# Optimization experiments

Measured on AMD Instinct MI355X. Metric: run time of the kernel, lower is better.

## Reference

```python
import jax, jax.numpy as jnp
import numpy as np
from itertools import combinations

H_RANK_MAX = 2
SELF_TP_RANK_MAX = 2
BASIS_RANK_MAX = 2
N_NODES = 25000
N_EDGES = 200000
N_CHANNELS = 32
DIM = 3
LETTERS = 'abdfghijklmn'  # avoid 'e' (edge) and 'c' (channel)


def _pairings(idxs):
    # all perfect matchings of a list of leg positions
    if not idxs:
        yield []
        return
    a = idxs[0]
    for i in range(1, len(idxs)):
        rest = idxs[1:i] + idxs[i + 1:]
        for p in _pairings(rest):
            yield [(a, idxs[i])] + p


def _contraction_subs(n_in, n_out):
    # all ways to keep n_out free legs (order-preserving) and pair up the rest
    specs = []
    for free in combinations(range(n_in), n_out):
        rest = [i for i in range(n_in) if i not in free]
        for match in _pairings(rest):
            sub = [None] * n_in
            out = ''
            li = 0
            for f in free:
                sub[f] = LETTERS[li]; out += LETTERS[li]; li += 1
            for x, y in match:
                sub[x] = sub[y] = LETTERS[li]; li += 1
            specs.append((''.join(sub), out))
    return specs


def _find_combinations(a_max, b_max, s):
    if s > a_max + b_max or s < 0:
        return []
    return [(a, s - a) for a in range(max(0, s - b_max), min(a_max, s) + 1)]


def setup_inputs() -> dict:
    key = jax.random.key(0)
    ks = jax.random.split(key, 9)
    return {
        'h0': jax.random.normal(ks[0], (N_NODES, N_CHANNELS), dtype=jnp.float32),
        'h1': jax.random.normal(ks[1], (N_NODES, N_CHANNELS, DIM), dtype=jnp.float32),
        'h2': jax.random.normal(ks[2], (N_NODES, N_CHANNELS, DIM, DIM), dtype=jnp.float32),
        'rel_pos': jax.random.normal(ks[3], (N_EDGES, DIM), dtype=jnp.float32),
        'edge_attr0': jax.random.normal(ks[4], (N_EDGES,), dtype=jnp.float32),
        'edge_attr1': jax.random.normal(ks[5], (N_EDGES, DIM), dtype=jnp.float32),
        'edge_attr2': jax.random.normal(ks[6], (N_EDGES, DIM, DIM), dtype=jnp.float32),
        'channel_weights': jax.random.normal(ks[7], (H_RANK_MAX + 1, N_CHANNELS, N_CHANNELS), dtype=jnp.float32),
        'edge_index': jax.random.randint(ks[8], (2, N_EDGES), 0, N_NODES, dtype=jnp.int64 if jax.config.jax_enable_x64 else jnp.int32),
    }


def _forward(h0, h1, h2, edge_attr0, edge_attr1, edge_attr2, channel_weights, edge_index):
    h = [h0, h1, h2]
    attr = [edge_attr0, edge_attr1, edge_attr2]
    recv = edge_index[1]
    # gather per-edge features and mix channels: [E, C, 3^r]
    h = [jnp.einsum('ij,kj...->ki...', channel_weights[r], h[r][recv])
         for r in range(H_RANK_MAX + 1)]
    acc = [None] * (BASIS_RANK_MAX + 1)
    for n_idx in range(H_RANK_MAX + SELF_TP_RANK_MAX + 1):
        for a, b in _find_combinations(H_RANK_MAX, SELF_TP_RANK_MAX, n_idx):
            for br in range(BASIS_RANK_MAX + 1):
                if n_idx >= br and (n_idx - br) % 2 == 0:
                    for sub, out in _contraction_subs(n_idx, br):
                        # contract outer(h[a], attr[b]) down to br free Cartesian legs
                        t = jnp.einsum(f'ec{sub[:a]},e{sub[a:]}->ec{out}', h[a], attr[b])
                        acc[br] = t if acc[br] is None else acc[br] + t
    send = edge_index[0]
    # scatter-sum per-edge messages into nodes
    return tuple(jax.ops.segment_sum(acc[br], send, num_segments=N_NODES)
                 for br in range(BASIS_RANK_MAX + 1))


def reference(h0, h1, h2, rel_pos, edge_attr0, edge_attr1, edge_attr2, channel_weights, edge_index):
    # rel_pos is accepted (matches original forward signature) but unused by the math
    return _forward(h0, h1, h2, edge_attr0, edge_attr1, edge_attr2, channel_weights, edge_index)
```

## Files before the change

kernel.cpp:

```cpp
#include <hip/hip_runtime.h>

#define N_NODES 25000
#define N_EDGES 200000
#define NC 32
#define DMAX 64

typedef unsigned int u32;
typedef u32   u32x4 __attribute__((ext_vector_type(4)));
typedef u32   u32x2 __attribute__((ext_vector_type(2)));
typedef float f32x2 __attribute__((ext_vector_type(2)));
typedef float f32x4 __attribute__((ext_vector_type(4)));
typedef u32x4 u32x4_a4 __attribute__((aligned(4)));
typedef u32x2 u32x2_a4 __attribute__((aligned(4)));
typedef f32x2 f32x2_a4 __attribute__((aligned(4)));
typedef f32x4 f32x4_a4 __attribute__((aligned(4)));

static constexpr size_t HM_BYTES   = (size_t)N_NODES * NC * 28;
static constexpr size_t SLOTS_OFF  = HM_BYTES;
static constexpr size_t CURSOR_OFF = SLOTS_OFF + (size_t)N_NODES * DMAX * 8;
static constexpr size_t WS_NEEDED  = CURSOR_OFF + (size_t)N_NODES * 4;

__device__ __forceinline__ unsigned short f2b(float f) {
    union { float f; unsigned u; } v; v.f = f;
    unsigned r = v.u + 0x7FFFu + ((v.u >> 16) & 1u);
    return (unsigned short)(r >> 16);
}
__device__ __forceinline__ float blo(u32 u) { return __uint_as_float(u << 16); }
__device__ __forceinline__ float bhi(u32 u) { return __uint_as_float(u & 0xFFFF0000u); }

__device__ __forceinline__ void edge_contract_g(
    float G, const float H1v[3], const float H2v[9],
    float a0, const float a1[3], const float a2[9],
    float& acc0, float acc1[3], float acc2[9])
{
    const float t2 = a2[0] + a2[4] + a2[8];
    const float s  = a0 + t2;

    float sA[9], S2[9];
#pragma unroll
    for (int a = 0; a < 3; ++a)
#pragma unroll
        for (int b = 0; b < 3; ++b) {
            sA[a*3+b] = a2[a*3+b] + a2[b*3+a];
            S2[a*3+b] = H2v[a*3+b] + H2v[b*3+a];
        }

    float v0 = G * s;
#pragma unroll
    for (int a = 0; a < 3; ++a) v0 += H1v[a] * a1[a];
#pragma unroll
    for (int k = 0; k < 9; ++k) v0 += H2v[k] * sA[k];
    acc0 += v0;

#pragma unroll
    for (int a = 0; a < 3; ++a) {
        float v = G * a1[a] + H1v[a] * s;
#pragma unroll
        for (int b = 0; b < 3; ++b)
            v += sA[a*3+b] * H1v[b] + S2[a*3+b] * a1[b];
        acc1[a] += v;
    }

#pragma unroll
    for (int a = 0; a < 3; ++a)
#pragma unroll
        for (int b = 0; b < 3; ++b) {
            float v = G * a2[a*3+b] + H1v[a] * a1[b] + H2v[a*3+b] * s;
#pragma unroll
            for (int d = 0; d < 3; ++d)
                v += S2[a*3+d] * sA[d*3+b];
            acc2[a*3+b] += v;
        }
}

__device__ __forceinline__ void edge_contract(
    float H0v, const float H1v[3], const float H2v[9],
    float a0, const float a1[3], const float a2[9],
    float& acc0, float acc1[3], float acc2[9])
{
    const float T2 = H2v[0] + H2v[4] + H2v[8];
    edge_contract_g(H0v + T2, H1v, H2v, a0, a1, a2, acc0, acc1, acc2);
}

__global__ __launch_bounds__(256) void mixscatter_kernel(
    const float* __restrict__ h0, const float* __restrict__ h1,
    const float* __restrict__ h2, const float* __restrict__ W,
    const int* __restrict__ ei,
    char* __restrict__ Hm, int2* __restrict__ slots, int* __restrict__ cursor)
{
    const int tid = threadIdx.x;

    if (blockIdx.x >= 3125) {
        const int e = (blockIdx.x - 3125) * 256 + tid;
        if (e < N_EDGES) {
            const int send = ei[e];
            const int pos  = atomicAdd(&cursor[send], 1);
            if (pos < DMAX) {
                int2 sl; sl.x = e; sl.y = ei[N_EDGES + e];
                slots[send * DMAX + pos] = sl;
            }
        }
        return;
    }

    __shared__ float Wt[3 * 32 * 32];
    __shared__ __align__(16) float h_lds[8 * 512];

    const int n0 = blockIdx.x * 8;

#pragma unroll
    for (int k = 0; k < 12; ++k) {
        int q = tid + k * 256;
        int r = q >> 10;
        int j = (q >> 5) & 31;
        int i = q & 31;
        Wt[q] = W[r * 1024 + i * 32 + j];
    }

    {
        int idx = tid;
        h_lds[(idx >> 5) * 512 + (idx & 31) * 16 + 0] = h0[(size_t)n0 * 32 + idx];
    }
#pragma unroll
    for (int k = 0; k < 3; ++k) {
        int idx = tid + k * 256;
        int ln = idx / 96, rem = idx % 96;
        h_lds[ln * 512 + (rem / 3) * 16 + 1 + (rem % 3)] = h1[(size_t)n0 * 96 + idx];
    }
#pragma unroll
    for (int k = 0; k < 9; ++k) {
        int idx = tid + k * 256;
        int ln = idx / 288, rem = idx % 288;
        h_lds[ln * 512 + (rem / 9) * 16 + 4 + (rem % 9)] = h2[(size_t)n0 * 288 + idx];
    }
    __syncthreads();

    const int ln = tid >> 5;
    const int i  = tid & 31;
    const int n  = n0 + ln;

    float acc[13];
#pragma unroll
    for (int p = 0; p < 13; ++p) acc[p] = 0.f;

#pragma unroll 4
    for (int j = 0; j < 32; ++j) {
        const float w0 = Wt[          j * 32 + i];
        const float w1 = Wt[1024 +    j * 32 + i];
        const float w2 = Wt[2048 +    j * 32 + i];
        const float* hv = &h_lds[ln * 512 + j * 16];
        const f32x4 qa = *(const f32x4*)(hv);
        const f32x4 qb = *(const f32x4*)(hv + 4);
        const f32x4 qc = *(const f32x4*)(hv + 8);
        const float hc = hv[12];
        acc[0]  += w0 * qa.x;
        acc[1]  += w1 * qa.y;  acc[2]  += w1 * qa.z;  acc[3]  += w1 * qa.w;
        acc[4]  += w2 * qb.x;  acc[5]  += w2 * qb.y;  acc[6]  += w2 * qb.z;
        acc[7]  += w2 * qb.w;  acc[8]  += w2 * qc.x;  acc[9]  += w2 * qc.y;
        acc[10] += w2 * qc.z;  acc[11] += w2 * qc.w;  acc[12] += w2 * hc;
    }

    acc[0] += acc[4] + acc[8] + acc[12];

    unsigned short b[13];
#pragma unroll
    for (int p = 0; p < 13; ++p) b[p] = f2b(acc[p]);
    u32 w0 = (u32)b[0]  | ((u32)b[1]  << 16);
    u32 w1 = (u32)b[2]  | ((u32)b[3]  << 16);
    u32 w2 = (u32)b[4]  | ((u32)b[5]  << 16);
    u32 w3 = (u32)b[6]  | ((u32)b[7]  << 16);
    u32 w4 = (u32)b[8]  | ((u32)b[9]  << 16);
    u32 w5 = (u32)b[10] | ((u32)b[11] << 16);
    u32 w6 = (u32)b[12];

    char* dst = Hm + (size_t)n * 896 + i * 28;
    u32x4 q0; q0.x = w0; q0.y = w1; q0.z = w2; q0.w = w3;
    u32x2 q1; q1.x = w4; q1.y = w5;
    *(u32x4_a4*)dst        = q0;
    *(u32x2_a4*)(dst + 16) = q1;
    *(u32*)(dst + 24)      = w6;
}

__global__ __launch_bounds__(128) void gather_kernel(
    const char* __restrict__ Hm, const int2* __restrict__ slots,
    const int* __restrict__ cursor,
    const float* __restrict__ ea0, const float* __restrict__ ea1,
    const float* __restrict__ ea2,
    float* __restrict__ out0, float* __restrict__ out1, float* __restrict__ out2)
{
    const int n    = blockIdx.x * 2 + (threadIdx.x >> 6);
    const int lane = threadIdx.x & 63;
    const int c    = lane & 31;
    const int par  = lane >> 5;

    const int draw = cursor[n];
    const int d    = draw < DMAX ? draw : DMAX;
    const int2* sb = slots + (u32)n * DMAX;
    const u32 c28  = (u32)c * 28u;

    const int2 my_sl = sb[lane];

    float acc0 = 0.f, acc1[3] = {0.f, 0.f, 0.f};
    float acc2[9] = {0.f, 0.f, 0.f, 0.f, 0.f, 0.f, 0.f, 0.f, 0.f};

#pragma unroll 2
    for (int i = par; i < d; i += 2) {
        const u32 e    = (u32)__shfl(my_sl.x, i);
        const u32 recv = (u32)__shfl(my_sl.y, i);

        const char* hmp = Hm + (recv * 896u + c28);
        const u32x4 q0 = *(const u32x4_a4*)hmp;
        const u32x2 q1 = *(const u32x2_a4*)(hmp + 16);
        const u32   q2 = *(const u32*)(hmp + 24);

        const float Gv = blo(q0.x);
        float H1v[3], H2v[9];
        H1v[0] = bhi(q0.x); H1v[1] = blo(q0.y); H1v[2] = bhi(q0.y);
        H2v[0] = blo(q0.z); H2v[1] = bhi(q0.z); H2v[2] = blo(q0.w);
        H2v[3] = bhi(q0.w); H2v[4] = blo(q1.x); H2v[5] = bhi(q1.x);
        H2v[6] = blo(q1.y); H2v[7] = bhi(q1.y); H2v[8] = blo(q2);

        const float a0 = ea0[e];
        float a1[3], a2[9];
        {
            const f32x2 v = *(const f32x2_a4*)(ea1 + e * 3u);
            a1[0] = v.x; a1[1] = v.y; a1[2] = ea1[e * 3u + 2u];
            const f32x4 b0 = *(const f32x4_a4*)(ea2 + e * 9u);
            const f32x4 b1 = *(const f32x4_a4*)(ea2 + e * 9u + 4u);
            a2[0] = b0.x; a2[1] = b0.y; a2[2] = b0.z; a2[3] = b0.w;
            a2[4] = b1.x; a2[5] = b1.y; a2[6] = b1.z; a2[7] = b1.w;
            a2[8] = ea2[e * 9u + 8u];
        }

        edge_contract_g(Gv, H1v, H2v, a0, a1, a2, acc0, acc1, acc2);
    }

    acc0 += __shfl_xor(acc0, 32);
#pragma unroll
    for (int a = 0; a < 3; ++a) acc1[a] += __shfl_xor(acc1[a], 32);
#pragma unroll
    for (int k = 0; k < 9; ++k) acc2[k] += __shfl_xor(acc2[k], 32);

    if (par == 0) {
        const u32 base = (u32)n * 32u + (u32)c;
        out0[base] = acc0;
        f32x2 o1; o1.x = acc1[0]; o1.y = acc1[1];
        *(f32x2_a4*)(out1 + base * 3u) = o1;
        out1[base * 3u + 2u] = acc1[2];
        f32x4 oa; oa.x = acc2[0]; oa.y = acc2[1]; oa.z = acc2[2]; oa.w = acc2[3];
        f32x4 ob; ob.x = acc2[4]; ob.y = acc2[5]; ob.z = acc2[6]; ob.w = acc2[7];
        *(f32x4_a4*)(out2 + base * 9u)      = oa;
        *(f32x4_a4*)(out2 + base * 9u + 4u) = ob;
        out2[base * 9u + 8u] = acc2[8];
    }
}

__global__ __launch_bounds__(256) void fused_edge_kernel(
    const float* __restrict__ h0, const float* __restrict__ h1,
    const float* __restrict__ h2, const float* __restrict__ W,
    const float* __restrict__ ea0, const float* __restrict__ ea1,
    const float* __restrict__ ea2, const int* __restrict__ ei,
    float* __restrict__ out0, float* __restrict__ out1, float* __restrict__ out2)
{
    __shared__ float Wt[3 * 32 * 32];
    __shared__ float h_lds[8 * 417];

    const int tid = threadIdx.x;
#pragma unroll
    for (int k = 0; k < 12; ++k) {
        int q = tid + k * 256;
        int r = q >> 10;
        int j = (q >> 5) & 31;
        int i = q & 31;
        Wt[q] = W[r * 1024 + i * 32 + j];
    }

    const int g = tid >> 5;
    const int c = tid & 31;
    const int e = blockIdx.x * 8 + g;
    const int send = ei[e];
    const int recv = ei[N_EDGES + e];

    h_lds[g * 417 + c * 13 + 0] = h0[(size_t)recv * 32 + c];
#pragma unroll
    for (int a = 0; a < 3; ++a)
        h_lds[g * 417 + c * 13 + 1 + a] = h1[(size_t)recv * 96 + c * 3 + a];
#pragma unroll
    for (int k = 0; k < 9; ++k)
        h_lds[g * 417 + c * 13 + 4 + k] = h2[(size_t)recv * 288 + c * 9 + k];
    __syncthreads();

    float acc[13];
#pragma unroll
    for (int p = 0; p < 13; ++p) acc[p] = 0.f;
#pragma unroll 4
    for (int j = 0; j < 32; ++j) {
        const float w0 = Wt[          j * 32 + c];
        const float w1 = Wt[1024 +    j * 32 + c];
        const float w2 = Wt[2048 +    j * 32 + c];
        const float* hv = &h_lds[g * 417 + j * 13];
        acc[0] += w0 * hv[0];
#pragma unroll
        for (int p = 0; p < 3; ++p) acc[1 + p] += w1 * hv[1 + p];
#pragma unroll
        for (int p = 0; p < 9; ++p) acc[4 + p] += w2 * hv[4 + p];
    }

    const float a0 = ea0[e];
    float a1[3], a2[9];
#pragma unroll
    for (int a = 0; a < 3; ++a) a1[a] = ea1[(size_t)e * 3 + a];
#pragma unroll
    for (int k = 0; k < 9; ++k) a2[k] = ea2[(size_t)e * 9 + k];

    float acc0 = 0.f, acc1[3] = {0.f, 0.f, 0.f};
    float acc2[9] = {0.f, 0.f, 0.f, 0.f, 0.f, 0.f, 0.f, 0.f, 0.f};
    edge_contract(acc[0], &acc[1], &acc[4], a0, a1, a2, acc0, acc1, acc2);

    const size_t base = (size_t)send * 32 + c;
    atomicAdd(out0 + base, acc0);
#pragma unroll
    for (int a = 0; a < 3; ++a) atomicAdd(out1 + base * 3 + a, acc1[a]);
#pragma unroll
    for (int k = 0; k < 9; ++k) atomicAdd(out2 + base * 9 + k, acc2[k]);
}

extern "C" void kernel_launch(void* const* d_in, const int* in_sizes, int n_in,
                              void* d_out, int out_size, void* d_ws, size_t ws_size,
                              hipStream_t stream) {
    const float* h0  = (const float*)d_in[0];
    const float* h1  = (const float*)d_in[1];
    const float* h2  = (const float*)d_in[2];
    const float* ea0 = (const float*)d_in[4];
    const float* ea1 = (const float*)d_in[5];
    const float* ea2 = (const float*)d_in[6];
    const float* W   = (const float*)d_in[7];
    const int*   ei  = (const int*)d_in[8];

    float* out0 = (float*)d_out;
    float* out1 = out0 + (size_t)N_NODES * 32;
    float* out2 = out1 + (size_t)N_NODES * 32 * 3;

    char* ws = (char*)d_ws;

    if (ws_size >= WS_NEEDED) {
        char* Hm     = ws;
        int2* slots  = (int2*)(ws + SLOTS_OFF);
        int*  cursor = (int*)(ws + CURSOR_OFF);

        hipMemsetAsync(cursor, 0, (size_t)N_NODES * 4, stream);
        mixscatter_kernel<<<3125 + 782, 256, 0, stream>>>(
            h0, h1, h2, W, ei, Hm, slots, cursor);
        gather_kernel<<<N_NODES / 2, 128, 0, stream>>>(
            Hm, slots, cursor, ea0, ea1, ea2, out0, out1, out2);
    } else {
        hipMemsetAsync(d_out, 0, (size_t)out_size * sizeof(float), stream);
        fused_edge_kernel<<<N_EDGES / 8, 256, 0, stream>>>(
            h0, h1, h2, W, ea0, ea1, ea2, ei, out0, out1, out2);
    }
}
```

Measured before the change: 90.00 us.

## Mix 16 nodes per block with two channels per thread; nontemporal gather loads

The channel-mixing part of mixscatter now handles 16 nodes per block, and each thread computes two output channels (i and i+16). This halves the number of W tile loads into LDS per node and reuses each LDS read of h across two channels, at the cost of more registers per thread. A bounds guard covers the partial final block. Separately, the gather kernel reads cursor, slots and edge attributes through nontemporal loads so these streamed values do not displace the reused Hm rows from cache.

```diff
diff --git a/kernel.cpp b/kernel.cpp
--- a/kernel.cpp
+++ b/kernel.cpp
@@ -4,6 +4,7 @@
 #define N_EDGES 200000
 #define NC 32
 #define DMAX 64
+#define MIXB 1563
 
 typedef unsigned int u32;
 typedef u32   u32x4 __attribute__((ext_vector_type(4)));
@@ -90,8 +91,8 @@
 {
     const int tid = threadIdx.x;
 
-    if (blockIdx.x >= 3125) {
-        const int e = (blockIdx.x - 3125) * 256 + tid;
+    if (blockIdx.x >= MIXB) {
+        const int e = (blockIdx.x - MIXB) * 256 + tid;
         if (e < N_EDGES) {
             const int send = ei[e];
             const int pos  = atomicAdd(&cursor[send], 1);
@@ -104,9 +105,10 @@
     }
 
     __shared__ float Wt[3 * 32 * 32];
-    __shared__ __align__(16) float h_lds[8 * 512];
-
-    const int n0 = blockIdx.x * 8;
+    __shared__ __align__(16) float h_lds[16 * 512];
+
+    const int n0     = blockIdx.x * 16;
+    const int nvalid = (N_NODES - n0 < 16) ? (N_NODES - n0) : 16;
 
 #pragma unroll
     for (int k = 0; k < 12; ++k) {
@@ -117,68 +119,93 @@
         Wt[q] = W[r * 1024 + i * 32 + j];
     }
 
-    {
-        int idx = tid;
-        h_lds[(idx >> 5) * 512 + (idx & 31) * 16 + 0] = h0[(size_t)n0 * 32 + idx];
-    }
-#pragma unroll
-    for (int k = 0; k < 3; ++k) {
+#pragma unroll
+    for (int k = 0; k < 2; ++k) {
         int idx = tid + k * 256;
-        int ln = idx / 96, rem = idx % 96;
-        h_lds[ln * 512 + (rem / 3) * 16 + 1 + (rem % 3)] = h1[(size_t)n0 * 96 + idx];
-    }
-#pragma unroll
-    for (int k = 0; k < 9; ++k) {
+        int node = idx >> 5, j = idx & 31;
+        if (node < nvalid)
+            h_lds[node * 512 + j * 16 + 0] = h0[(size_t)n0 * 32 + idx];
+    }
+#pragma unroll
+    for (int k = 0; k < 6; ++k) {
         int idx = tid + k * 256;
-        int ln = idx / 288, rem = idx % 288;
-        h_lds[ln * 512 + (rem / 9) * 16 + 4 + (rem % 9)] = h2[(size_t)n0 * 288 + idx];
+        int node = idx / 96, rem = idx % 96;
+        if (node < nvalid)
+            h_lds[node * 512 + (rem / 3) * 16 + 1 + (rem % 3)] = h1[(size_t)n0 * 96 + idx];
+    }
+#pragma unroll
+    for (int k = 0; k < 18; ++k) {
+        int idx = tid + k * 256;
+        int node = idx / 288, rem = idx % 288;
+        if (node < nvalid)
+            h_lds[node * 512 + (rem / 9) * 16 + 4 + (rem % 9)] = h2[(size_t)n0 * 288 + idx];
     }
     __syncthreads();
 
-    const int ln = tid >> 5;
-    const int i  = tid & 31;
+    const int ln = tid >> 4;
+    const int i  = tid & 15;
     const int n  = n0 + ln;
-
-    float acc[13];
-#pragma unroll
-    for (int p = 0; p < 13; ++p) acc[p] = 0.f;
-
-#pragma unroll 4
+    if (ln >= nvalid) return;
+
+    float accA[13], accB[13];
+#pragma unroll
+    for (int p = 0; p < 13; ++p) { accA[p] = 0.f; accB[p] = 0.f; }
+
+#pragma unroll 2
     for (int j = 0; j < 32; ++j) {
-        const float w0 = Wt[          j * 32 + i];
-        const float w1 = Wt[1024 +    j * 32 + i];
-        const float w2 = Wt[2048 +    j * 32 + i];
+        const float w0a = Wt[          j * 32 + i];
+        const float w0b = Wt[          j * 32 + i + 16];
+        const float w1a = Wt[1024 +    j * 32 + i];
+        const float w1b = Wt[1024 +    j * 32 + i + 16];
+        const float w2a = Wt[2048 +    j * 32 + i];
+        const float w2b = Wt[2048 +    j * 32 + i + 16];
         const float* hv = &h_lds[ln * 512 + j * 16];
         const f32x4 qa = *(const f32x4*)(hv);
         const f32x4 qb = *(const f32x4*)(hv + 4);
         const f32x4 qc = *(const f32x4*)(hv + 8);
         const float hc = hv[12];
-        acc[0]  += w0 * qa.x;
-        acc[1]  += w1 * qa.y;  acc[2]  += w1 * qa.z;  acc[3]  += w1 * qa.w;
-        acc[4]  += w2 * qb.x;  acc[5]  += w2 * qb.y;  acc[6]  += w2 * qb.z;
-        acc[7]  += w2 * qb.w;  acc[8]  += w2 * qc.x;  acc[9]  += w2 * qc.y;
-        acc[10] += w2 * qc.z;  acc[11] += w2 * qc.w;  acc[12] += w2 * hc;
-    }
-
-    acc[0] += acc[4] + acc[8] + acc[12];
-
-    unsigned short b[13];
-#pragma unroll
-    for (int p = 0; p < 13; ++p) b[p] = f2b(acc[p]);
-    u32 w0 = (u32)b[0]  | ((u32)b[1]  << 16);
-    u32 w1 = (u32)b[2]  | ((u32)b[3]  << 16);
-    u32 w2 = (u32)b[4]  | ((u32)b[5]  << 16);
-    u32 w3 = (u32)b[6]  | ((u32)b[7]  << 16);
-    u32 w4 = (u32)b[8]  | ((u32)b[9]  << 16);
-    u32 w5 = (u32)b[10] | ((u32)b[11] << 16);
-    u32 w6 = (u32)b[12];
-
-    char* dst = Hm + (size_t)n * 896 + i * 28;
-    u32x4 q0; q0.x = w0; q0.y = w1; q0.z = w2; q0.w = w3;
-    u32x2 q1; q1.x = w4; q1.y = w5;
-    *(u32x4_a4*)dst        = q0;
-    *(u32x2_a4*)(dst + 16) = q1;
-    *(u32*)(dst + 24)      = w6;
+        accA[0]  += w0a * qa.x;                      accB[0]  += w0b * qa.x;
+        accA[1]  += w1a * qa.y;                      accB[1]  += w1b * qa.y;
+        accA[2]  += w1a * qa.z;                      accB[2]  += w1b * qa.z;
+        accA[3]  += w1a * qa.w;                      accB[3]  += w1b * qa.w;
+        accA[4]  += w2a * qb.x;                      accB[4]  += w2b * qb.x;
+        accA[5]  += w2a * qb.y;                      accB[5]  += w2b * qb.y;
+        accA[6]  += w2a * qb.z;                      accB[6]  += w2b * qb.z;
+        accA[7]  += w2a * qb.w;                      accB[7]  += w2b * qb.w;
+        accA[8]  += w2a * qc.x;                      accB[8]  += w2b * qc.x;
+        accA[9]  += w2a * qc.y;                      accB[9]  += w2b * qc.y;
+        accA[10] += w2a * qc.z;                      accB[10] += w2b * qc.z;
+        accA[11] += w2a * qc.w;                      accB[11] += w2b * qc.w;
+        accA[12] += w2a * hc;                        accB[12] += w2b * hc;
+    }
+
+    accA[0] += accA[4] + accA[8] + accA[12];
+    accB[0] += accB[4] + accB[8] + accB[12];
+
+    {
+        unsigned short b[13];
+#pragma unroll
+        for (int p = 0; p < 13; ++p) b[p] = f2b(accA[p]);
+        u32x4 q0; q0.x = (u32)b[0] | ((u32)b[1] << 16); q0.y = (u32)b[2] | ((u32)b[3] << 16);
+        q0.z = (u32)b[4] | ((u32)b[5] << 16); q0.w = (u32)b[6] | ((u32)b[7] << 16);
+        u32x2 q1; q1.x = (u32)b[8] | ((u32)b[9] << 16); q1.y = (u32)b[10] | ((u32)b[11] << 16);
+        char* dst = Hm + (size_t)n * 896 + i * 28;
+        *(u32x4_a4*)dst        = q0;
+        *(u32x2_a4*)(dst + 16) = q1;
+        *(u32*)(dst + 24)      = (u32)b[12];
+    }
+    {
+        unsigned short b[13];
+#pragma unroll
+        for (int p = 0; p < 13; ++p) b[p] = f2b(accB[p]);
+        u32x4 q0; q0.x = (u32)b[0] | ((u32)b[1] << 16); q0.y = (u32)b[2] | ((u32)b[3] << 16);
+        q0.z = (u32)b[4] | ((u32)b[5] << 16); q0.w = (u32)b[6] | ((u32)b[7] << 16);
+        u32x2 q1; q1.x = (u32)b[8] | ((u32)b[9] << 16); q1.y = (u32)b[10] | ((u32)b[11] << 16);
+        char* dst = Hm + (size_t)n * 896 + (i + 16) * 28;
+        *(u32x4_a4*)dst        = q0;
+        *(u32x2_a4*)(dst + 16) = q1;
+        *(u32*)(dst + 24)      = (u32)b[12];
+    }
 }
 
 __global__ __launch_bounds__(128) void gather_kernel(
@@ -193,20 +220,20 @@
     const int c    = lane & 31;
     const int par  = lane >> 5;
 
-    const int draw = cursor[n];
+    const int draw = __builtin_nontemporal_load(cursor + n);
     const int d    = draw < DMAX ? draw : DMAX;
-    const int2* sb = slots + (u32)n * DMAX;
     const u32 c28  = (u32)c * 28u;
 
-    const int2 my_sl = sb[lane];
+    const u32x2 my_sl = __builtin_nontemporal_load(
+        (const u32x2_a4*)(slots + (u32)n * DMAX + lane));
 
     float acc0 = 0.f, acc1[3] = {0.f, 0.f, 0.f};
     float acc2[9] = {0.f, 0.f, 0.f, 0.f, 0.f, 0.f, 0.f, 0.f, 0.f};
 
 #pragma unroll 2
     for (int i = par; i < d; i += 2) {
-        const u32 e    = (u32)__shfl(my_sl.x, i);
-        const u32 recv = (u32)__shfl(my_sl.y, i);
+        const u32 e    = (u32)__shfl((int)my_sl.x, i);
+        const u32 recv = (u32)__shfl((int)my_sl.y, i);
 
         const char* hmp = Hm + (recv * 896u + c28);
         const u32x4 q0 = *(const u32x4_a4*)hmp;
@@ -220,16 +247,17 @@
         H2v[3] = bhi(q0.w); H2v[4] = blo(q1.x); H2v[5] = bhi(q1.x);
         H2v[6] = blo(q1.y); H2v[7] = bhi(q1.y); H2v[8] = blo(q2);
 
-        const float a0 = ea0[e];
+        const float a0 = __builtin_nontemporal_load(ea0 + e);
         float a1[3], a2[9];
         {
-            const f32x2 v = *(const f32x2_a4*)(ea1 + e * 3u);
-            a1[0] = v.x; a1[1] = v.y; a1[2] = ea1[e * 3u + 2u];
-            const f32x4 b0 = *(const f32x4_a4*)(ea2 + e * 9u);
-            const f32x4 b1 = *(const f32x4_a4*)(ea2 + e * 9u + 4u);
+            const f32x2 v = __builtin_nontemporal_load((const f32x2_a4*)(ea1 + e * 3u));
+            a1[0] = v.x; a1[1] = v.y;
+            a1[2] = __builtin_nontemporal_load(ea1 + e * 3u + 2u);
+            const f32x4 b0 = __builtin_nontemporal_load((const f32x4_a4*)(ea2 + e * 9u));
+            const f32x4 b1 = __builtin_nontemporal_load((const f32x4_a4*)(ea2 + e * 9u + 4u));
             a2[0] = b0.x; a2[1] = b0.y; a2[2] = b0.z; a2[3] = b0.w;
             a2[4] = b1.x; a2[5] = b1.y; a2[6] = b1.z; a2[7] = b1.w;
-            a2[8] = ea2[e * 9u + 8u];
+            a2[8] = __builtin_nontemporal_load(ea2 + e * 9u + 8u);
         }
 
         edge_contract_g(Gv, H1v, H2v, a0, a1, a2, acc0, acc1, acc2);
@@ -349,7 +377,7 @@
         int*  cursor = (int*)(ws + CURSOR_OFF);
 
         hipMemsetAsync(cursor, 0, (size_t)N_NODES * 4, stream);
-        mixscatter_kernel<<<3125 + 782, 256, 0, stream>>>(
+        mixscatter_kernel<<<MIXB + 782, 256, 0, stream>>>(
             h0, h1, h2, W, ei, Hm, slots, cursor);
         gather_kernel<<<N_NODES / 2, 128, 0, stream>>>(
             Hm, slots, cursor, ea0, ea1, ea2, out0, out1, out2);
```

New measurement: 112.2 us. +24.6%, slower.
